# Optimization experiments

Measured on AMD Instinct MI355X. Metric: run time of the kernel, lower is better.

## Reference

```python
import jax, jax.numpy as jnp
import numpy as np

B, S, DIN, D, H, DK, FF, V, L = 4, 1024, 768, 224, 8, 28, 600, 8000, 8


def setup_inputs() -> dict:
    key = jax.random.key(0)
    ks = iter(jax.random.split(key, 32))
    g = lambda shape, s=0.02: jax.random.normal(next(ks), shape, jnp.float32) * s
    return {
        "x": jax.random.normal(next(ks), (B, S, DIN), jnp.float32),
        "Wp": g((DIN, D)), "bp": jnp.zeros((D,), jnp.float32),
        # per-layer stacked params, leading axis = L layers
        "Wq": g((L, H, D, DK)), "bq": jnp.zeros((L, H, DK), jnp.float32),
        "Wk": g((L, H, D, DK)), "bk": jnp.zeros((L, H, DK), jnp.float32),
        "Wv": g((L, H, D, DK)), "bv": jnp.zeros((L, H, DK), jnp.float32),
        "Wo": g((L, D, D)), "bo": jnp.zeros((L, D), jnp.float32),
        "W1": g((L, D, FF)), "b1": jnp.zeros((L, FF), jnp.float32),
        "W2": g((L, FF, FF)), "b2": jnp.zeros((L, FF), jnp.float32),
        "W3": g((L, FF, D)), "b3": jnp.zeros((L, D), jnp.float32),
        # LayerNorm over last TWO dims (seq, dmodel), one shared instance per layer
        "lnw": jnp.ones((L, S, D), jnp.float32), "lnb": jnp.zeros((L, S, D), jnp.float32),
        "Wf": g((D, V)), "bf": jnp.zeros((V,), jnp.float32),
    }


def _pos_enc(S_, D_):
    pos = jnp.arange(S_, dtype=jnp.float32)[:, None]          # [S,1]
    i = jnp.arange(D_, dtype=jnp.float32)[None, :]            # [1,D]
    ang = pos / jnp.power(jnp.float32(10000.0), 2.0 * i / D_)  # uses 2*i for BOTH
    return jnp.where(jnp.arange(D_)[None, :] % 2 == 0, jnp.sin(ang), jnp.cos(ang))


def _ln2d(x, w, b):
    # LayerNorm over last two dims (seq, dmodel), eps=1e-5
    mu = jnp.mean(x, axis=(-2, -1), keepdims=True)
    var = jnp.var(x, axis=(-2, -1), keepdims=True)
    return (x - mu) / jnp.sqrt(var + 1e-5) * w + b


def _attn(x, Wq, bq, Wk, bk, Wv, bv, Wo, bo):
    q = jnp.einsum('bsd,hdk->bhsk', x, Wq) + bq[:, None, :]
    k = jnp.einsum('bsd,hdk->bhsk', x, Wk) + bk[:, None, :]
    v = jnp.einsum('bsd,hdk->bhsk', x, Wv) + bv[:, None, :]
    scores = jnp.einsum('bhqk,bhsk->bhqs', q, k) / jnp.sqrt(jnp.float32(DK))
    causal = jnp.tril(jnp.ones((S, S), bool))
    scores = jnp.where(causal, scores, -jnp.inf)
    a = jax.nn.softmax(scores, axis=-1)
    o = jnp.einsum('bhqs,bhsk->bqhk', a, v).reshape(x.shape[0], S, D)
    return o @ Wo + bo + x  # residual inside attention (as in source)


def reference(x, Wp, bp, Wq, bq, Wk, bk, Wv, bv, Wo, bo,
              W1, b1, W2, b2, W3, b3, lnw, lnb, Wf, bf):
    h = x @ Wp + bp                      # proj_to_224: [B,S,224]
    h = h + _pos_enc(S, D)[None]         # positional encoding
    for l in range(L):
        h = _attn(h, Wq[l], bq[l], Wk[l], bk[l], Wv[l], bv[l], Wo[l], bo[l])
        h = _ln2d(h, lnw[l], lnb[l])
        f = jax.nn.relu(h @ W1[l] + b1[l])
        f = jax.nn.relu(f @ W2[l] + b2[l])
        f = f @ W3[l] + b3[l]
        h = _ln2d(f + h, lnw[l], lnb[l])  # feed_forward's LN (same params)
        h = _ln2d(h, lnw[l], lnb[l])      # outer LN (same params again)
    logits = (h @ Wf + bf) / 1.0          # temperature = 1.0
    return jax.nn.softmax(logits, axis=2)
```

## Files before the change

### kernel.cpp

```cpp
#include <hip/hip_runtime.h>
#include <math.h>

#define GF_BIAS   1
#define GF_RELU   2
#define GF_RESID  4
#define GF_POSENC 8
#define GF_F32OUT 16
#define GF_STAT6  32
#define GF_SWAP   64
#define GF_LNA    128
#define GF_LNA2   256
#define GF_LNRES  512
#define GF_LNRES2 1024

namespace {
constexpr int BB = 4, SS = 1024, DD = 224, FFF = 600, VV = 8000, LLl = 8;
constexpr int SD = SS * DD;
constexpr float INV_SD = 1.0f / (float)SD;

constexpr size_t WP   = 0;
constexpr size_t WQKV = WP + (size_t)256 * 768;
constexpr size_t WO   = WQKV + (size_t)LLl * 704 * 256;
constexpr size_t W1T  = WO + (size_t)LLl * 256 * 256;
constexpr size_t W2T  = W1T + (size_t)LLl * 640 * 256;
constexpr size_t W3T  = W2T + (size_t)LLl * 640 * 640;
constexpr size_t WFT  = W3T + (size_t)LLl * 256 * 640;
constexpr size_t HB   = WFT + (size_t)8064 * 256;
constexpr size_t H2B  = HB + (size_t)4096 * 256;
constexpr size_t OBUF = H2B + (size_t)4096 * 256;
constexpr size_t BIG  = OBUF + (size_t)4096 * 256;
constexpr size_t ENDB = BIG + (size_t)2 * 4096 * 640;
constexpr size_t FBYTE = ENDB * 2;
}

using short8 = __attribute__((ext_vector_type(8))) short;
using f32x4  = __attribute__((ext_vector_type(4))) float;

__device__ __forceinline__ float bits2f(unsigned u) {
  union { unsigned u; float f; } v; v.u = u; return v.f;
}
__device__ __forceinline__ unsigned short f2b(float f) {
  union { float f; unsigned u; } v; v.f = f;
  unsigned r = v.u + 0x7FFFu + ((v.u >> 16) & 1u);
  return (unsigned short)(r >> 16);
}
__device__ __forceinline__ float b2f(unsigned short b) {
  return bits2f((unsigned)b << 16);
}

__device__ __forceinline__ uint4 ln8(uint4 raw, const float* __restrict__ wp,
                                     const float* __restrict__ bp,
                                     float mu1, float rs1, float mu2, float rs2,
                                     bool dbl) {
  float4 w0 = *(const float4*)wp, w1v = *(const float4*)(wp + 4);
  float4 b0 = *(const float4*)bp, b1v = *(const float4*)(bp + 4);
  float wv[8] = {w0.x, w0.y, w0.z, w0.w, w1v.x, w1v.y, w1v.z, w1v.w};
  float bv[8] = {b0.x, b0.y, b0.z, b0.w, b1v.x, b1v.y, b1v.z, b1v.w};
  const unsigned* u = (const unsigned*)&raw;
  uint4 out;
  unsigned* ou = (unsigned*)&out;
#pragma unroll
  for (int q = 0; q < 4; ++q) {
    float x0 = bits2f(u[q] << 16), x1 = bits2f(u[q] & 0xFFFF0000u);
    float y0 = (x0 - mu1) * rs1 * wv[q * 2] + bv[q * 2];
    float y1 = (x1 - mu1) * rs1 * wv[q * 2 + 1] + bv[q * 2 + 1];
    if (dbl) {
      y0 = (y0 - mu2) * rs2 * wv[q * 2] + bv[q * 2];
      y1 = (y1 - mu2) * rs2 * wv[q * 2 + 1] + bv[q * 2 + 1];
    }
    ou[q] = (unsigned)f2b(y0) | ((unsigned)f2b(y1) << 16);
  }
  return out;
}

template <int BM, int BN, int FLAGS>
__global__ __launch_bounds__(256) void gemm_mfma(
    const unsigned short* __restrict__ A, const unsigned short* __restrict__ Bt,
    const float* __restrict__ bias, const unsigned short* __restrict__ Rz,
    void* __restrict__ Cout, int Kp, int N, int ldc,
    const float* __restrict__ lnwT, const float* __restrict__ lnbT,
    const float* __restrict__ stIn, const float* __restrict__ cst,
    const float* __restrict__ lnwS, const float* __restrict__ lnbS,
    float* __restrict__ statOut)
{
  constexpr bool HASLNA = (FLAGS & (GF_LNA | GF_LNA2)) != 0;
  constexpr bool HASLNR = (FLAGS & (GF_LNRES | GF_LNRES2)) != 0;
  constexpr bool DBLA = (FLAGS & GF_LNA2) != 0;
  constexpr bool DBLR = (FLAGS & GF_LNRES2) != 0;
  constexpr int MR = BM / 32, NR = BN / 32;
  constexpr int APT = BM / 32, BPT = BN / 32;
  constexpr int ABY = BM * 128, BBY = BN * 128;
  constexpr int CBY = (FLAGS & GF_F32OUT) ? (64 * (BN + 4) * 4) : (BM * (BN + 8) * 2);
  constexpr int SBY = (ABY + BBY) > CBY ? (ABY + BBY) : CBY;
  __shared__ __align__(16) char smem[SBY];
  __shared__ float red6[24];
  unsigned short* sA = (unsigned short*)smem;
  unsigned short* sB = (unsigned short*)(smem + ABY);
  const int t = threadIdx.x;
  const int l = t & 63;
  const int w = t >> 6, wr = w >> 1, wc = w & 1;
  const int m0 = ((FLAGS & GF_SWAP) ? blockIdx.x : blockIdx.y) * BM;
  const int n0 = ((FLAGS & GF_SWAP) ? blockIdx.y : blockIdx.x) * BN;
  const int nk = Kp >> 6;

  float mu1 = 0.f, rs1 = 1.f, mu2 = 0.f, rs2 = 1.f;
  if constexpr (HASLNA || HASLNR) {
    const float* st = stIn + (m0 >> 10) * 6;
    const float s0 = st[0], s1 = st[1];
    mu1 = s0 * INV_SD;
    rs1 = rsqrtf(s1 * INV_SD - mu1 * mu1 + 1e-5f);
    if constexpr (DBLA || DBLR) {
      const float swx = st[2], sw2x = st[3], sw2x2 = st[4], swbx = st[5];
      mu2 = (rs1 * (swx - mu1 * cst[0]) + cst[2]) * INV_SD;
      const float ey2 = (rs1 * rs1 * (sw2x2 - 2.f * mu1 * sw2x + mu1 * mu1 * cst[1]) +
                         2.f * rs1 * (swbx - mu1 * cst[4]) + cst[3]) * INV_SD;
      rs2 = rsqrtf(ey2 - mu2 * mu2 + 1e-5f);
    }
  }

  int aoff[APT], ar[APT], ac[APT];
#pragma unroll
  for (int p = 0; p < APT; ++p) {
    int off = (t + p * 256) * 16;
    int r = off >> 7;
    int cb = (off & 127) ^ ((r & 7) << 4);
    aoff[p] = off; ar[p] = r; ac[p] = cb >> 1;
  }
  int boff[BPT], br[BPT], bc[BPT];
#pragma unroll
  for (int p = 0; p < BPT; ++p) {
    int off = (t + p * 256) * 16;
    int r = off >> 7;
    int cb = (off & 127) ^ ((r & 7) << 4);
    boff[p] = off; br[p] = r; bc[p] = cb >> 1;
  }

  const unsigned short* Ab = A + (size_t)m0 * Kp;
  const unsigned short* Bb = Bt + (size_t)n0 * Kp;

  auto loadA = [&](int p, int kb) -> uint4 {
    const int d0 = kb + ac[p];
    uint4 raw = *(const uint4*)(Ab + (size_t)ar[p] * Kp + d0);
    if constexpr (HASLNA) {
      if (d0 >= DD) return make_uint4(0u, 0u, 0u, 0u);
      const int srow = (m0 + ar[p]) & (SS - 1);
      raw = ln8(raw, lnwT + (size_t)srow * DD + d0, lnbT + (size_t)srow * DD + d0,
                mu1, rs1, mu2, rs2, DBLA);
    }
    return raw;
  };

  uint4 ra[APT], rb[BPT];
#pragma unroll
  for (int p = 0; p < APT; ++p) ra[p] = loadA(p, 0);
#pragma unroll
  for (int p = 0; p < BPT; ++p) rb[p] = *(const uint4*)(Bb + (size_t)br[p] * Kp + bc[p]);

  f32x4 acc[MR][NR];
#pragma unroll
  for (int i = 0; i < MR; ++i)
#pragma unroll
    for (int j = 0; j < NR; ++j) acc[i][j] = {0.f, 0.f, 0.f, 0.f};

  for (int kt = 0; kt < nk; ++kt) {
#pragma unroll
    for (int p = 0; p < APT; ++p) *(uint4*)((char*)sA + aoff[p]) = ra[p];
#pragma unroll
    for (int p = 0; p < BPT; ++p) *(uint4*)((char*)sB + boff[p]) = rb[p];
    __syncthreads();
    if (kt + 1 < nk) {
      const int k1 = (kt + 1) * 64;
#pragma unroll
      for (int p = 0; p < APT; ++p) ra[p] = loadA(p, k1);
#pragma unroll
      for (int p = 0; p < BPT; ++p) rb[p] = *(const uint4*)(Bb + (size_t)br[p] * Kp + k1 + bc[p]);
    }
#pragma unroll
    for (int kh = 0; kh < 2; ++kh) {
      short8 af[MR], bfg[NR];
#pragma unroll
      for (int mi = 0; mi < MR; ++mi) {
        const int row = wr * (BM / 2) + mi * 16 + (l & 15);
        const int byte = (row * 128 + kh * 64 + (l >> 4) * 16) ^ ((row & 7) << 4);
        af[mi] = *(const short8*)((const char*)sA + byte);
      }
#pragma unroll
      for (int ni = 0; ni < NR; ++ni) {
        const int row = wc * (BN / 2) + ni * 16 + (l & 15);
        const int byte = (row * 128 + kh * 64 + (l >> 4) * 16) ^ ((row & 7) << 4);
        bfg[ni] = *(const short8*)((const char*)sB + byte);
      }
#pragma unroll
      for (int mi = 0; mi < MR; ++mi)
#pragma unroll
        for (int ni = 0; ni < NR; ++ni)
          acc[mi][ni] = __builtin_amdgcn_mfma_f32_16x16x32_bf16(af[mi], bfg[ni], acc[mi][ni], 0, 0, 0);
    }
    __syncthreads();
  }

  const int cl = l & 15, rl0 = (l >> 4) * 4;

  if constexpr ((FLAGS & GF_F32OUT) != 0) {
    constexpr int CST = BN + 4;
    float* Cs = (float*)smem;
    constexpr int NCH = BM / 64;
#pragma unroll
    for (int c = 0; c < NCH; ++c) {
      __syncthreads();
      if ((wr * (BM / 2)) / 64 == c) {
#pragma unroll
        for (int mi = 0; mi < MR; ++mi)
#pragma unroll
          for (int ni = 0; ni < NR; ++ni)
#pragma unroll
            for (int j = 0; j < 4; ++j) {
              const int rl = wr * (BM / 2) + mi * 16 + rl0 + j - c * 64;
              const int cc = wc * (BN / 2) + ni * 16 + cl;
              const int gn = n0 + cc;
              float v = acc[mi][ni][j];
              if ((FLAGS & GF_BIAS) && gn < N) v += bias[gn];
              Cs[rl * CST + cc] = v;
            }
      }
      __syncthreads();
      constexpr int CPR = BN / 4;
      constexpr int NIT = (64 * CPR) / 256;
#pragma unroll
      for (int i = 0; i < NIT; ++i) {
        const int ch = i * 256 + t;
        const int rr = ch / CPR, c4 = ch % CPR;
        const int gn = n0 + c4 * 4;
        const size_t gmr = (size_t)(m0 + c * 64 + rr);
        if (gn + 3 < N) {
          *(float4*)&((float*)Cout)[gmr * ldc + gn] = *(const float4*)&Cs[rr * CST + c4 * 4];
        } else {
#pragma unroll
          for (int c2 = 0; c2 < 4; ++c2)
            if (gn + c2 < N) ((float*)Cout)[gmr * ldc + gn + c2] = Cs[rr * CST + c4 * 4 + c2];
        }
      }
    }
  } else {
    constexpr int CST = BN + 8;
    unsigned short* Cs = (unsigned short*)smem;
    float ls0 = 0.f, ls1 = 0.f, ls2 = 0.f, ls3 = 0.f, ls4 = 0.f, ls5 = 0.f;
#pragma unroll
    for (int mi = 0; mi < MR; ++mi)
#pragma unroll
      for (int ni = 0; ni < NR; ++ni)
#pragma unroll
        for (int j = 0; j < 4; ++j) {
          const int rl = wr * (BM / 2) + mi * 16 + rl0 + j;
          const int cc = wc * (BN / 2) + ni * 16 + cl;
          const int gm = m0 + rl, gn = n0 + cc;
          const int srow = gm & (SS - 1);
          float v = acc[mi][ni][j];
          if ((FLAGS & GF_BIAS) && gn < N) v += bias[gn];
          if constexpr ((FLAGS & GF_RESID) != 0) {
            if constexpr (HASLNR) {
              if (gn < N) {
                float rv = b2f(Rz[(size_t)gm * ldc + gn]);
                const float wE = lnwT[(size_t)srow * DD + gn];
                const float bE = lnbT[(size_t)srow * DD + gn];
                rv = (rv - mu1) * rs1 * wE + bE;
                if constexpr (DBLR) rv = (rv - mu2) * rs2 * wE + bE;
                v += rv;
              }
            } else {
              v += b2f(Rz[(size_t)gm * ldc + gn]);
            }
          }
          if ((FLAGS & GF_POSENC) && gn < N) {
            float freq = expf(-(2.0f * gn / 224.0f) * 9.210340371976184f);
            float ang = (float)srow * freq;
            v += (gn & 1) ? cosf(ang) : sinf(ang);
          }
          if (FLAGS & GF_RELU) v = fmaxf(v, 0.f);
          if constexpr ((FLAGS & GF_STAT6) != 0) {
            if (gn < N) {
              const float wS = lnwS[(size_t)srow * DD + gn];
              const float bS = lnbS[(size_t)srow * DD + gn];
              const float wv = wS * v;
              ls0 += v; ls1 += v * v; ls2 += wv; ls3 += wS * wv;
              ls4 += wv * wv; ls5 += bS * wv;
            }
          }
          Cs[rl * CST + cc] = f2b(v);
        }
    __syncthreads();
#pragma unroll
    for (int it = 0; it < BM / 32; ++it) {
      const int rr = it * 32 + (t >> 3), qq = t & 7;
      const size_t gm = (size_t)(m0 + rr);
      *(uint4*)&((unsigned short*)Cout)[gm * ldc + n0 + qq * 8] =
          *(const uint4*)&Cs[rr * CST + qq * 8];
    }
    if constexpr ((FLAGS & GF_STAT6) != 0) {
      float s[6] = {ls0, ls1, ls2, ls3, ls4, ls5};
#pragma unroll
      for (int o2 = 32; o2 > 0; o2 >>= 1)
#pragma unroll
        for (int j = 0; j < 6; ++j) s[j] += __shfl_down(s[j], o2);
      if (l == 0)
#pragma unroll
        for (int j = 0; j < 6; ++j) red6[w * 6 + j] = s[j];
      __syncthreads();
      if (t < 6) {
        const float tot = red6[t] + red6[6 + t] + red6[12 + t] + red6[18 + t];
        atomicAdd(&statOut[(m0 >> 10) * 6 + t], tot);
      }
    }
  }
}

__global__ __launch_bounds__(512) void ffn_fused(
    const unsigned short* __restrict__ h2a,
    const unsigned short* __restrict__ W1t, const unsigned short* __restrict__ W2t,
    const unsigned short* __restrict__ W3t,
    const float* __restrict__ b1, const float* __restrict__ b2,
    const float* __restrict__ b3,
    const float* __restrict__ lnw, const float* __restrict__ lnb,
    const float* __restrict__ stA, float* __restrict__ statOut,
    unsigned short* __restrict__ Xout)
{
  __shared__ __align__(16) unsigned short sA[16 * 280];
  __shared__ __align__(16) unsigned short f1s[16 * 648];
  __shared__ __align__(16) unsigned short f2s[16 * 648];
  __shared__ float red6[48];
  const int t = threadIdx.x;
  const int l = t & 63, w = t >> 6;
  const int cl = l & 15, g8 = (l >> 4) * 8, rl0 = (l >> 4) * 4;
  const int m0 = blockIdx.x * 16;
  const float* st = stA + (m0 >> 10) * 6;
  const float mu1 = st[0] * INV_SD;
  const float rs1 = rsqrtf(st[1] * INV_SD - mu1 * mu1 + 1e-5f);

  {
    const int r = t >> 5, col = (t & 31) * 8;
    uint4 v = make_uint4(0u, 0u, 0u, 0u);
    if (col < DD) {
      const int srow = (m0 + r) & (SS - 1);
      uint4 raw = *(const uint4*)(h2a + (size_t)(m0 + r) * 256 + col);
      v = ln8(raw, lnw + (size_t)srow * DD + col, lnb + (size_t)srow * DD + col,
              mu1, rs1, 0.f, 1.f, false);
    }
    *(uint4*)(sA + r * 280 + col) = v;
  }
  __syncthreads();

  {
    f32x4 acc[5];
#pragma unroll
    for (int i = 0; i < 5; ++i) acc[i] = {0.f, 0.f, 0.f, 0.f};
    for (int ks = 0; ks < 8; ++ks) {
      const short8 af = *(const short8*)(sA + cl * 280 + ks * 32 + g8);
#pragma unroll
      for (int ni = 0; ni < 5; ++ni) {
        const int n = w * 80 + ni * 16 + cl;
        const short8 bf = *(const short8*)(W1t + (size_t)n * 256 + ks * 32 + g8);
        acc[ni] = __builtin_amdgcn_mfma_f32_16x16x32_bf16(af, bf, acc[ni], 0, 0, 0);
      }
    }
#pragma unroll
    for (int ni = 0; ni < 5; ++ni) {
      const int col = w * 80 + ni * 16 + cl;
      const float bias = (col < FFF) ? b1[col] : 0.f;
#pragma unroll
      for (int j = 0; j < 4; ++j)
        f1s[(rl0 + j) * 648 + col] = f2b(fmaxf(acc[ni][j] + bias, 0.f));
    }
  }
  __syncthreads();

  {
    f32x4 acc[5];
#pragma unroll
    for (int i = 0; i < 5; ++i) acc[i] = {0.f, 0.f, 0.f, 0.f};
    for (int ks = 0; ks < 20; ++ks) {
      const short8 af = *(const short8*)(f1s + cl * 648 + ks * 32 + g8);
#pragma unroll
      for (int ni = 0; ni < 5; ++ni) {
        const int n = w * 80 + ni * 16 + cl;
        const short8 bf = *(const short8*)(W2t + (size_t)n * 640 + ks * 32 + g8);
        acc[ni] = __builtin_amdgcn_mfma_f32_16x16x32_bf16(af, bf, acc[ni], 0, 0, 0);
      }
    }
#pragma unroll
    for (int ni = 0; ni < 5; ++ni) {
      const int col = w * 80 + ni * 16 + cl;
      const float bias = (col < FFF) ? b2[col] : 0.f;
#pragma unroll
      for (int j = 0; j < 4; ++j)
        f2s[(rl0 + j) * 648 + col] = f2b(fmaxf(acc[ni][j] + bias, 0.f));
    }
  }
  __syncthreads();

  float s6[6] = {0.f, 0.f, 0.f, 0.f, 0.f, 0.f};
  {
    f32x4 acc[2];
#pragma unroll
    for (int i = 0; i < 2; ++i) acc[i] = {0.f, 0.f, 0.f, 0.f};
    for (int ks = 0; ks < 20; ++ks) {
      const short8 af = *(const short8*)(f2s + cl * 648 + ks * 32 + g8);
#pragma unroll
      for (int ni = 0; ni < 2; ++ni) {
        const int n = w * 32 + ni * 16 + cl;
        const short8 bf = *(const short8*)(W3t + (size_t)n * 640 + ks * 32 + g8);
        acc[ni] = __builtin_amdgcn_mfma_f32_16x16x32_bf16(af, bf, acc[ni], 0, 0, 0);
      }
    }
    unsigned short* Cs = sA;
#pragma unroll
    for (int ni = 0; ni < 2; ++ni) {
      const int col = w * 32 + ni * 16 + cl;
      const float bias = (col < DD) ? b3[col] : 0.f;
#pragma unroll
      for (int j = 0; j < 4; ++j) {
        const int gm = m0 + rl0 + j;
        const int srow = gm & (SS - 1);
        float v = acc[ni][j] + bias;
        if (col < DD) {
          const float wE = lnw[(size_t)srow * DD + col];
          const float bE = lnb[(size_t)srow * DD + col];
          v += (b2f(h2a[(size_t)gm * 256 + col]) - mu1) * rs1 * wE + bE;
          const float wv = wE * v;
          s6[0] += v; s6[1] += v * v; s6[2] += wv; s6[3] += wE * wv;
          s6[4] += wv * wv; s6[5] += bE * wv;
        }
        Cs[(rl0 + j) * 280 + col] = f2b(v);
      }
    }
  }
#pragma unroll
  for (int o2 = 32; o2 > 0; o2 >>= 1)
#pragma unroll
    for (int j2 = 0; j2 < 6; ++j2) s6[j2] += __shfl_down(s6[j2], o2);
  if (l == 0)
#pragma unroll
    for (int j2 = 0; j2 < 6; ++j2) red6[w * 6 + j2] = s6[j2];
  __syncthreads();
  if (t < 6) {
    float tot = 0.f;
#pragma unroll
    for (int ww = 0; ww < 8; ++ww) tot += red6[ww * 6 + t];
    atomicAdd(&statOut[(m0 >> 10) * 6 + t], tot);
  }
  {
    const int r = t >> 5, col = (t & 31) * 8;
    *(uint4*)(Xout + (size_t)(m0 + r) * 256 + col) = *(const uint4*)(sA + r * 280 + col);
  }
}

__global__ __launch_bounds__(256) void ln2mat(
    const unsigned short* __restrict__ X, const float* __restrict__ lnw,
    const float* __restrict__ lnb, const float* __restrict__ st,
    const float* __restrict__ cst, unsigned short* __restrict__ Y)
{
  const int chunk = blockIdx.x * 256 + threadIdx.x;
  const int r = chunk >> 5, cc = chunk & 31;
  if (cc >= 28) {
    *(uint4*)(Y + (size_t)r * 256 + cc * 8) = make_uint4(0u, 0u, 0u, 0u);
    return;
  }
  const int b = r >> 10, srow = r & 1023;
  const float* s = st + b * 6;
  const float mu1 = s[0] * INV_SD;
  const float rs1 = rsqrtf(s[1] * INV_SD - mu1 * mu1 + 1e-5f);
  const float mu2 = (rs1 * (s[2] - mu1 * cst[0]) + cst[2]) * INV_SD;
  const float ey2 = (rs1 * rs1 * (s[4] - 2.f * mu1 * s[3] + mu1 * mu1 * cst[1]) +
                     2.f * rs1 * (s[5] - mu1 * cst[4]) + cst[3]) * INV_SD;
  const float rs2 = rsqrtf(ey2 - mu2 * mu2 + 1e-5f);
  uint4 raw = *(const uint4*)(X + (size_t)r * 256 + cc * 8);
  uint4 out = ln8(raw, lnw + (size_t)srow * DD + cc * 8, lnb + (size_t)srow * DD + cc * 8,
                  mu1, rs1, mu2, rs2, true);
  *(uint4*)(Y + (size_t)r * 256 + cc * 8) = out;
}

__device__ __forceinline__ void prep_wt2_body(
    const float* __restrict__ W, unsigned short* __restrict__ O,
    int K, int N, int Kp, int Np, size_t sW, size_t sO, int tile, int ll,
    float* __restrict__ T )
{
  const int tx = Np >> 5;
  const int tn = tile % tx, tk = tile / tx;
  const int n0 = tn * 32, k0 = tk * 32;
  const float* Wl = W + sW * ll;
  unsigned short* Ol = O + sO * ll;
  {
    const int r = threadIdx.x >> 3, c4 = (threadIdx.x & 7) * 4;
    const int k = k0 + r, n = n0 + c4;
    float4 v = make_float4(0.f, 0.f, 0.f, 0.f);
    if (k < K) {
      if (n + 3 < N) v = *(const float4*)&Wl[(size_t)k * N + n];
      else {
        if (n + 0 < N) v.x = Wl[(size_t)k * N + n + 0];
        if (n + 1 < N) v.y = Wl[(size_t)k * N + n + 1];
        if (n + 2 < N) v.z = Wl[(size_t)k * N + n + 2];
        if (n + 3 < N) v.w = Wl[(size_t)k * N + n + 3];
      }
    }
    *(float4*)&T[r * 36 + c4] = v;
  }
  __syncthreads();
  {
    const int nl = threadIdx.x >> 3, k4 = (threadIdx.x & 7) * 4;
    ushort4 u;
    u.x = f2b(T[(k4 + 0) * 36 + nl]); u.y = f2b(T[(k4 + 1) * 36 + nl]);
    u.z = f2b(T[(k4 + 2) * 36 + nl]); u.w = f2b(T[(k4 + 3) * 36 + nl]);
    *(ushort4*)&Ol[(size_t)(n0 + nl) * Kp + k0 + k4] = u;
  }
}

__global__ __launch_bounds__(256) void prep_weights(
    const float* __restrict__ Wp, const float* __restrict__ Wo,
    const float* __restrict__ W1, const float* __restrict__ W2,
    const float* __restrict__ W3, const float* __restrict__ Wf,
    const float* __restrict__ lnw, const float* __restrict__ lnb,
    unsigned short* __restrict__ wpT, unsigned short* __restrict__ woT,
    unsigned short* __restrict__ w1T, unsigned short* __restrict__ w2T,
    unsigned short* __restrict__ w3T, unsigned short* __restrict__ wfT,
    float* __restrict__ cst)
{
  __shared__ float T[32 * 36];
  const int b = blockIdx.x;
  if (b < 192) {
    prep_wt2_body(Wp, wpT, 768, 224, 768, 256, 0, 0, b, 0, T);
  } else if (b < 704) {
    const int f = b - 192;
    prep_wt2_body(Wo, woT, 224, 224, 256, 256, (size_t)224 * 224, (size_t)256 * 256,
                  f % 64, f / 64, T);
  } else if (b < 1984) {
    const int f = b - 704;
    prep_wt2_body(W1, w1T, 224, 600, 256, 640, (size_t)224 * 600, (size_t)640 * 256,
                  f % 160, f / 160, T);
  } else if (b < 5184) {
    const int f = b - 1984;
    prep_wt2_body(W2, w2T, 600, 600, 640, 640, (size_t)600 * 600, (size_t)640 * 640,
                  f % 400, f / 400, T);
  } else if (b < 6464) {
    const int f = b - 5184;
    prep_wt2_body(W3, w3T, 600, 224, 640, 256, (size_t)600 * 224, (size_t)256 * 640,
                  f % 160, f / 160, T);
  } else if (b < 8480) {
    prep_wt2_body(Wf, wfT, 224, 8000, 256, 8064, 0, 0, b - 6464, 0, T);
  } else {
    const int f = b - 8480;
    const int g = f & 63, ll = f >> 6;
    const float* wv = lnw + (size_t)ll * SD + g * 3584;
    const float* bv = lnb + (size_t)ll * SD + g * 3584;
    float s[5] = {0.f, 0.f, 0.f, 0.f, 0.f};
    for (int c = threadIdx.x * 4; c < 3584; c += 1024) {
      float4 w4 = *(const float4*)(wv + c);
      float4 b4 = *(const float4*)(bv + c);
      const float* wf2 = (const float*)&w4;
// ... 170 lines not shown
    const int row = qbase + g * 4 + jj;
    unsigned short* op = o + ((size_t)(b * SS + row)) * 256 + h * 28;
    op[cl] = f2b(o0[jj] * inv);
    if (cl < 12) op[16 + cl] = f2b(o1[jj] * inv);
  }
}

__global__ __launch_bounds__(256) void softmax_rows(float* __restrict__ logits)
{
  const int row = blockIdx.x;
  float* p = logits + (size_t)row * VV;
  __shared__ float4 buf[VV / 4];
  __shared__ float red[4];
  const int tid = threadIdx.x;

  float mx = -INFINITY;
  for (int i = tid; i < VV / 4; i += 256) {
    float4 v = *(const float4*)(p + i * 4);
    buf[i] = v;
    mx = fmaxf(fmaxf(fmaxf(mx, v.x), fmaxf(v.y, v.z)), v.w);
  }
#pragma unroll
  for (int o2 = 32; o2 > 0; o2 >>= 1) mx = fmaxf(mx, __shfl_down(mx, o2));
  if ((tid & 63) == 0) red[tid >> 6] = mx;
  __syncthreads();
  mx = fmaxf(fmaxf(red[0], red[1]), fmaxf(red[2], red[3]));
  __syncthreads();

  float s = 0.f;
  for (int i = tid; i < VV / 4; i += 256) {
    float4 v = buf[i];
    v.x = __expf(v.x - mx); v.y = __expf(v.y - mx);
    v.z = __expf(v.z - mx); v.w = __expf(v.w - mx);
    buf[i] = v;
    s += v.x + v.y + v.z + v.w;
  }
#pragma unroll
  for (int o2 = 32; o2 > 0; o2 >>= 1) s += __shfl_down(s, o2);
  if ((tid & 63) == 0) red[tid >> 6] = s;
  __syncthreads();
  s = red[0] + red[1] + red[2] + red[3];
  const float inv = 1.0f / s;
  for (int i = tid; i < VV / 4; i += 256) {
    float4 v = buf[i];
    v.x *= inv; v.y *= inv; v.z *= inv; v.w *= inv;
    *(float4*)(p + i * 4) = v;
  }
}

extern "C" void kernel_launch(void* const* d_in, const int* in_sizes, int n_in,
                              void* d_out, int out_size, void* d_ws, size_t ws_size,
                              hipStream_t stream) {
  const float* x   = (const float*)d_in[0];
  const float* Wp  = (const float*)d_in[1];
  const float* bp  = (const float*)d_in[2];
  const float* Wq  = (const float*)d_in[3];
  const float* bq  = (const float*)d_in[4];
  const float* Wk  = (const float*)d_in[5];
  const float* bk  = (const float*)d_in[6];
  const float* Wv  = (const float*)d_in[7];
  const float* bv  = (const float*)d_in[8];
  const float* Wo  = (const float*)d_in[9];
  const float* bo  = (const float*)d_in[10];
  const float* W1  = (const float*)d_in[11];
  const float* b1  = (const float*)d_in[12];
  const float* W2  = (const float*)d_in[13];
  const float* b2  = (const float*)d_in[14];
  const float* W3  = (const float*)d_in[15];
  const float* b3  = (const float*)d_in[16];
  const float* lnw = (const float*)d_in[17];
  const float* lnb = (const float*)d_in[18];
  const float* Wf  = (const float*)d_in[19];
  const float* bf  = (const float*)d_in[20];

  unsigned short* wsb = (unsigned short*)d_ws;
  unsigned short* wpT   = wsb + WP;
  unsigned short* wqkvT = wsb + WQKV;
  unsigned short* woT   = wsb + WO;
  unsigned short* w1T   = wsb + W1T;
  unsigned short* w2T   = wsb + W2T;
  unsigned short* w3T   = wsb + W3T;
  unsigned short* wfT   = wsb + WFT;
  unsigned short* X     = wsb + HB;
  unsigned short* h2a   = wsb + H2B;
  unsigned short* obuf  = wsb + OBUF;
  unsigned short* xb    = wsb + BIG;
  unsigned short* qkvb  = wsb + BIG;
  float* bcat  = (float*)((char*)d_ws + FBYTE);
  float* stats = bcat + LLl * 672;
  float* cstA  = stats + 384;

  hipMemsetAsync(wqkvT, 0, (size_t)LLl * 704 * 256 * 2, stream);
  prep_x<<<3072, 256, 0, stream>>>(x, xb, stats);
  prep_wqkv<<<1568, 256, 0, stream>>>(Wq, Wk, Wv, bq, bk, bv, wqkvT, bcat);
  prep_weights<<<8992, 256, 0, stream>>>(Wp, Wo, W1, W2, W3, Wf, lnw, lnb,
                                         wpT, woT, w1T, w2T, w3T, wfT, cstA);

  gemm_mfma<32, 64, GF_BIAS | GF_POSENC><<<dim3(4, 128), 256, 0, stream>>>(
      xb, wpT, bp, nullptr, X, 768, 224, 256,
      nullptr, nullptr, nullptr, nullptr, nullptr, nullptr, nullptr);

  for (int l = 0; l < LLl; ++l) {
    float* stA = stats + (size_t)(2 * l) * 24;
    float* stB = stats + (size_t)(2 * l + 1) * 24;
    const float* stPrev = stats + (size_t)(2 * l - 1) * 24;
    const float* lnwP = lnw + (size_t)(l - 1) * SD;
    const float* lnbP = lnb + (size_t)(l - 1) * SD;
    const float* cstP = cstA + (l - 1) * 5;
    const float* lnwL = lnw + (size_t)l * SD;
    const float* lnbL = lnb + (size_t)l * SD;

    if (l == 0) {
      gemm_mfma<64, 64, GF_BIAS><<<dim3(11, 64), 256, 0, stream>>>(
          X, wqkvT, bcat, nullptr, qkvb, 256, 672, 704,
          nullptr, nullptr, nullptr, nullptr, nullptr, nullptr, nullptr);
    } else {
      gemm_mfma<64, 64, GF_BIAS | GF_LNA2><<<dim3(11, 64), 256, 0, stream>>>(
          X, wqkvT + (size_t)l * 704 * 256, bcat + l * 672, nullptr, qkvb, 256, 672, 704,
          lnwP, lnbP, stPrev, cstP, nullptr, nullptr, nullptr);
    }
    attn_mfma<<<dim3(BB * 8, SS / 64), 256, 0, stream>>>(qkvb, obuf);
    if (l == 0) {
      gemm_mfma<32, 64, GF_BIAS | GF_RESID | GF_STAT6><<<dim3(4, 128), 256, 0, stream>>>(
          obuf, woT, bo, X, h2a, 256, 224, 256,
          nullptr, nullptr, nullptr, nullptr, lnwL, lnbL, stA);
    } else {
      gemm_mfma<32, 64, GF_BIAS | GF_RESID | GF_LNRES2 | GF_STAT6>
          <<<dim3(4, 128), 256, 0, stream>>>(
          obuf, woT + (size_t)l * 256 * 256, bo + (size_t)l * 224, X, h2a, 256, 224, 256,
          lnwP, lnbP, stPrev, cstP, lnwL, lnbL, stA);
    }
    ffn_fused<<<256, 512, 0, stream>>>(
        h2a, w1T + (size_t)l * 640 * 256, w2T + (size_t)l * 640 * 640,
        w3T + (size_t)l * 256 * 640, b1 + (size_t)l * 600, b2 + (size_t)l * 600,
        b3 + (size_t)l * 224, lnwL, lnbL, stA, stB, X);
  }

  ln2mat<<<512, 256, 0, stream>>>(X, lnw + (size_t)7 * SD, lnb + (size_t)7 * SD,
                                  stats + (size_t)15 * 24, cstA + 7 * 5, h2a);
  gemm_mfma<128, 128, GF_BIAS | GF_F32OUT | GF_SWAP><<<dim3(32, 63), 256, 0, stream>>>(
      h2a, wfT, bf, nullptr, (float*)d_out, 256, 8000, 8000,
      nullptr, nullptr, nullptr, nullptr, nullptr, nullptr, nullptr);
  softmax_rows<<<4096, 256, 0, stream>>>((float*)d_out);
}
```

Baseline: 1.250 ms.

## Fuse out-projection, FFN and next-layer QKV into one cooperative kernel per layer

Replaces the per-layer out-projection GEMM, the FFN kernel and the next layer's QKV GEMM with a single cooperative kernel. It uses grid-wide syncs to wait for the LayerNorm statistics between stages, and keeps the intermediate h2a tile in shared memory instead of global memory. This removes two kernel launches per layer and a global round trip of the intermediate activation. In exchange, 256 blocks of 512 threads must be co-resident, each grid.sync costs a barrier, and the out-projection and QKV stages run on only 16-row tiles with weights read straight from global memory.

Measured after the change: 1.722 ms. 1.38x slower.

```diff
diff --git a/kernel.cpp b/kernel.cpp
--- a/kernel.cpp
+++ b/kernel.cpp
@@ -1,17 +1,15 @@
 #include <hip/hip_runtime.h>
+#include <hip/hip_cooperative_groups.h>
 #include <math.h>
+
+namespace cg = cooperative_groups;
 
 #define GF_BIAS   1
 #define GF_RELU   2
 #define GF_RESID  4
 #define GF_POSENC 8
 #define GF_F32OUT 16
-#define GF_STAT6  32
 #define GF_SWAP   64
-#define GF_LNA    128
-#define GF_LNA2   256
-#define GF_LNRES  512
-#define GF_LNRES2 1024
 
 namespace {
 constexpr int BB = 4, SS = 1024, DD = 224, FFF = 600, VV = 8000, LLl = 8;
@@ -73,27 +71,29 @@
   return out;
 }
 
+__device__ __forceinline__ void ln2stats(const float* __restrict__ st,
+                                         const float* __restrict__ cst,
+                                         float& mu1, float& rs1, float& mu2, float& rs2)
+{
+  mu1 = st[0] * INV_SD;
+  rs1 = rsqrtf(st[1] * INV_SD - mu1 * mu1 + 1e-5f);
+  mu2 = (rs1 * (st[2] - mu1 * cst[0]) + cst[2]) * INV_SD;
+  const float ey2 = (rs1 * rs1 * (st[4] - 2.f * mu1 * st[3] + mu1 * mu1 * cst[1]) +
+                     2.f * rs1 * (st[5] - mu1 * cst[4]) + cst[3]) * INV_SD;
+  rs2 = rsqrtf(ey2 - mu2 * mu2 + 1e-5f);
+}
+
 template <int BM, int BN, int FLAGS>
 __global__ __launch_bounds__(256) void gemm_mfma(
     const unsigned short* __restrict__ A, const unsigned short* __restrict__ Bt,
-    const float* __restrict__ bias, const unsigned short* __restrict__ Rz,
-    void* __restrict__ Cout, int Kp, int N, int ldc,
-    const float* __restrict__ lnwT, const float* __restrict__ lnbT,
-    const float* __restrict__ stIn, const float* __restrict__ cst,
-    const float* __restrict__ lnwS, const float* __restrict__ lnbS,
-    float* __restrict__ statOut)
+    const float* __restrict__ bias, void* __restrict__ Cout, int Kp, int N, int ldc)
 {
-  constexpr bool HASLNA = (FLAGS & (GF_LNA | GF_LNA2)) != 0;
-  constexpr bool HASLNR = (FLAGS & (GF_LNRES | GF_LNRES2)) != 0;
-  constexpr bool DBLA = (FLAGS & GF_LNA2) != 0;
-  constexpr bool DBLR = (FLAGS & GF_LNRES2) != 0;
   constexpr int MR = BM / 32, NR = BN / 32;
   constexpr int APT = BM / 32, BPT = BN / 32;
   constexpr int ABY = BM * 128, BBY = BN * 128;
   constexpr int CBY = (FLAGS & GF_F32OUT) ? (64 * (BN + 4) * 4) : (BM * (BN + 8) * 2);
   constexpr int SBY = (ABY + BBY) > CBY ? (ABY + BBY) : CBY;
   __shared__ __align__(16) char smem[SBY];
-  __shared__ float red6[24];
   unsigned short* sA = (unsigned short*)smem;
   unsigned short* sB = (unsigned short*)(smem + ABY);
   const int t = threadIdx.x;
@@ -103,21 +103,6 @@
   const int n0 = ((FLAGS & GF_SWAP) ? blockIdx.y : blockIdx.x) * BN;
   const int nk = Kp >> 6;
 
-  float mu1 = 0.f, rs1 = 1.f, mu2 = 0.f, rs2 = 1.f;
-  if constexpr (HASLNA || HASLNR) {
-    const float* st = stIn + (m0 >> 10) * 6;
-    const float s0 = st[0], s1 = st[1];
-    mu1 = s0 * INV_SD;
-    rs1 = rsqrtf(s1 * INV_SD - mu1 * mu1 + 1e-5f);
-    if constexpr (DBLA || DBLR) {
-      const float swx = st[2], sw2x = st[3], sw2x2 = st[4], swbx = st[5];
-      mu2 = (rs1 * (swx - mu1 * cst[0]) + cst[2]) * INV_SD;
-      const float ey2 = (rs1 * rs1 * (sw2x2 - 2.f * mu1 * sw2x + mu1 * mu1 * cst[1]) +
-                         2.f * rs1 * (swbx - mu1 * cst[4]) + cst[3]) * INV_SD;
-      rs2 = rsqrtf(ey2 - mu2 * mu2 + 1e-5f);
-    }
-  }
-
   int aoff[APT], ar[APT], ac[APT];
 #pragma unroll
   for (int p = 0; p < APT; ++p) {
@@ -138,21 +123,9 @@
   const unsigned short* Ab = A + (size_t)m0 * Kp;
   const unsigned short* Bb = Bt + (size_t)n0 * Kp;
 
-  auto loadA = [&](int p, int kb) -> uint4 {
-    const int d0 = kb + ac[p];
-    uint4 raw = *(const uint4*)(Ab + (size_t)ar[p] * Kp + d0);
-    if constexpr (HASLNA) {
-      if (d0 >= DD) return make_uint4(0u, 0u, 0u, 0u);
-      const int srow = (m0 + ar[p]) & (SS - 1);
-      raw = ln8(raw, lnwT + (size_t)srow * DD + d0, lnbT + (size_t)srow * DD + d0,
-                mu1, rs1, mu2, rs2, DBLA);
-    }
-    return raw;
-  };
-
   uint4 ra[APT], rb[BPT];
 #pragma unroll
-  for (int p = 0; p < APT; ++p) ra[p] = loadA(p, 0);
+  for (int p = 0; p < APT; ++p) ra[p] = *(const uint4*)(Ab + (size_t)ar[p] * Kp + ac[p]);
 #pragma unroll
   for (int p = 0; p < BPT; ++p) rb[p] = *(const uint4*)(Bb + (size_t)br[p] * Kp + bc[p]);
 
@@ -171,7 +144,7 @@
     if (kt + 1 < nk) {
       const int k1 = (kt + 1) * 64;
 #pragma unroll
-      for (int p = 0; p < APT; ++p) ra[p] = loadA(p, k1);
+      for (int p = 0; p < APT; ++p) ra[p] = *(const uint4*)(Ab + (size_t)ar[p] * Kp + k1 + ac[p]);
 #pragma unroll
       for (int p = 0; p < BPT; ++p) rb[p] = *(const uint4*)(Bb + (size_t)br[p] * Kp + k1 + bc[p]);
     }
@@ -244,7 +217,6 @@
   } else {
     constexpr int CST = BN + 8;
     unsigned short* Cs = (unsigned short*)smem;
-    float ls0 = 0.f, ls1 = 0.f, ls2 = 0.f, ls3 = 0.f, ls4 = 0.f, ls5 = 0.f;
 #pragma unroll
     for (int mi = 0; mi < MR; ++mi)
 #pragma unroll
@@ -257,35 +229,11 @@
           const int srow = gm & (SS - 1);
           float v = acc[mi][ni][j];
           if ((FLAGS & GF_BIAS) && gn < N) v += bias[gn];
-          if constexpr ((FLAGS & GF_RESID) != 0) {
-            if constexpr (HASLNR) {
-              if (gn < N) {
-                float rv = b2f(Rz[(size_t)gm * ldc + gn]);
-                const float wE = lnwT[(size_t)srow * DD + gn];
-                const float bE = lnbT[(size_t)srow * DD + gn];
-                rv = (rv - mu1) * rs1 * wE + bE;
-                if constexpr (DBLR) rv = (rv - mu2) * rs2 * wE + bE;
-                v += rv;
-              }
-            } else {
-              v += b2f(Rz[(size_t)gm * ldc + gn]);
-            }
-          }
           if ((FLAGS & GF_POSENC) && gn < N) {
             float freq = expf(-(2.0f * gn / 224.0f) * 9.210340371976184f);
             float ang = (float)srow * freq;
             v += (gn & 1) ? cosf(ang) : sinf(ang);
           }
-          if (FLAGS & GF_RELU) v = fmaxf(v, 0.f);
-          if constexpr ((FLAGS & GF_STAT6) != 0) {
-            if (gn < N) {
-              const float wS = lnwS[(size_t)srow * DD + gn];
-              const float bS = lnbS[(size_t)srow * DD + gn];
-              const float wv = wS * v;
-              ls0 += v; ls1 += v * v; ls2 += wv; ls3 += wS * wv;
-              ls4 += wv * wv; ls5 += bS * wv;
-            }
-          }
           Cs[rl * CST + cc] = f2b(v);
         }
     __syncthreads();
@@ -296,160 +244,269 @@
       *(uint4*)&((unsigned short*)Cout)[gm * ldc + n0 + qq * 8] =
           *(const uint4*)&Cs[rr * CST + qq * 8];
     }
-    if constexpr ((FLAGS & GF_STAT6) != 0) {
-      float s[6] = {ls0, ls1, ls2, ls3, ls4, ls5};
-#pragma unroll
-      for (int o2 = 32; o2 > 0; o2 >>= 1)
-#pragma unroll
-        for (int j = 0; j < 6; ++j) s[j] += __shfl_down(s[j], o2);
-      if (l == 0)
-#pragma unroll
-        for (int j = 0; j < 6; ++j) red6[w * 6 + j] = s[j];
-      __syncthreads();
-      if (t < 6) {
-        const float tot = red6[t] + red6[6 + t] + red6[12 + t] + red6[18 + t];
-        atomicAdd(&statOut[(m0 >> 10) * 6 + t], tot);
-      }
-    }
-  }
-}
-
-__global__ __launch_bounds__(512) void ffn_fused(
-    const unsigned short* __restrict__ h2a,
+  }
+}
+
+__global__ __launch_bounds__(512) void layer_tail(
+    const unsigned short* __restrict__ obuf, unsigned short* __restrict__ X,
+    unsigned short* __restrict__ qkvb,
+    const unsigned short* __restrict__ woT, const float* __restrict__ bo,
     const unsigned short* __restrict__ W1t, const unsigned short* __restrict__ W2t,
     const unsigned short* __restrict__ W3t,
     const float* __restrict__ b1, const float* __restrict__ b2,
     const float* __restrict__ b3,
-    const float* __restrict__ lnw, const float* __restrict__ lnb,
-    const float* __restrict__ stA, float* __restrict__ statOut,
-    unsigned short* __restrict__ Xout)
+    const unsigned short* __restrict__ wqN, const float* __restrict__ bcN,
+    const float* __restrict__ lnwP, const float* __restrict__ lnbP,
+    const float* __restrict__ cstP, const float* __restrict__ stPrev,
+    const float* __restrict__ lnwL, const float* __restrict__ lnbL,
+    const float* __restrict__ cstL,
+    float* __restrict__ stA, float* __restrict__ stB,
+    int isL0, int hasQkv)
 {
-  __shared__ __align__(16) unsigned short sA[16 * 280];
-  __shared__ __align__(16) unsigned short f1s[16 * 648];
-  __shared__ __align__(16) unsigned short f2s[16 * 648];
-  __shared__ float red6[48];
+  cg::grid_group grid = cg::this_grid();
+  __shared__ __align__(16) char smem[59584];
+  unsigned short* oS   = (unsigned short*)smem;
+  unsigned short* sAx  = (unsigned short*)smem;
+  unsigned short* h2aL = (unsigned short*)(smem + 8960);
+  unsigned short* f1s  = (unsigned short*)(smem + 17920);
+  unsigned short* f2s  = (unsigned short*)(smem + 38656);
+  unsigned short* qS   = (unsigned short*)(smem + 17920);
+  float* red6 = (float*)(smem + 59392);
+
   const int t = threadIdx.x;
   const int l = t & 63, w = t >> 6;
   const int cl = l & 15, g8 = (l >> 4) * 8, rl0 = (l >> 4) * 4;
   const int m0 = blockIdx.x * 16;
-  const float* st = stA + (m0 >> 10) * 6;
-  const float mu1 = st[0] * INV_SD;
-  const float rs1 = rsqrtf(st[1] * INV_SD - mu1 * mu1 + 1e-5f);
+  const int batch = m0 >> 10;
+
+  float mu1 = 0.f, rs1 = 1.f, mu2 = 0.f, rs2 = 1.f;
+  if (!isL0) ln2stats(stPrev + batch * 6, cstP, mu1, rs1, mu2, rs2);
 
   {
     const int r = t >> 5, col = (t & 31) * 8;
-    uint4 v = make_uint4(0u, 0u, 0u, 0u);
-    if (col < DD) {
-      const int srow = (m0 + r) & (SS - 1);
-      uint4 raw = *(const uint4*)(h2a + (size_t)(m0 + r) * 256 + col);
-      v = ln8(raw, lnw + (size_t)srow * DD + col, lnb + (size_t)srow * DD + col,
-              mu1, rs1, 0.f, 1.f, false);
-    }
-    *(uint4*)(sA + r * 280 + col) = v;
+    *(uint4*)(oS + r * 280 + col) = *(const uint4*)(obuf + (size_t)(m0 + r) * 256 + col);
   }
   __syncthreads();
 
-  {
-    f32x4 acc[5];
-#pragma unroll
-    for (int i = 0; i < 5; ++i) acc[i] = {0.f, 0.f, 0.f, 0.f};
-    for (int ks = 0; ks < 8; ++ks) {
-      const short8 af = *(const short8*)(sA + cl * 280 + ks * 32 + g8);
-#pragma unroll
-      for (int ni = 0; ni < 5; ++ni) {
-        const int n = w * 80 + ni * 16 + cl;
-        const short8 bf = *(const short8*)(W1t + (size_t)n * 256 + ks * 32 + g8);
-        acc[ni] = __builtin_amdgcn_mfma_f32_16x16x32_bf16(af, bf, acc[ni], 0, 0, 0);
-      }
-    }
-#pragma unroll
-    for (int ni = 0; ni < 5; ++ni) {
-      const int col = w * 80 + ni * 16 + cl;
-      const float bias = (col < FFF) ? b1[col] : 0.f;
-#pragma unroll
-      for (int j = 0; j < 4; ++j)
-        f1s[(rl0 + j) * 648 + col] = f2b(fmaxf(acc[ni][j] + bias, 0.f));
-    }
-  }
-  __syncthreads();
-
-  {
-    f32x4 acc[5];
-#pragma unroll
-    for (int i = 0; i < 5; ++i) acc[i] = {0.f, 0.f, 0.f, 0.f};
-    for (int ks = 0; ks < 20; ++ks) {
-      const short8 af = *(const short8*)(f1s + cl * 648 + ks * 32 + g8);
-#pragma unroll
-      for (int ni = 0; ni < 5; ++ni) {
-        const int n = w * 80 + ni * 16 + cl;
-        const short8 bf = *(const short8*)(W2t + (size_t)n * 640 + ks * 32 + g8);
-        acc[ni] = __builtin_amdgcn_mfma_f32_16x16x32_bf16(af, bf, acc[ni], 0, 0, 0);
-      }
-    }
-#pragma unroll
-    for (int ni = 0; ni < 5; ++ni) {
-      const int col = w * 80 + ni * 16 + cl;
-      const float bias = (col < FFF) ? b2[col] : 0.f;
-#pragma unroll
-      for (int j = 0; j < 4; ++j)
-        f2s[(rl0 + j) * 648 + col] = f2b(fmaxf(acc[ni][j] + bias, 0.f));
-    }
-  }
-  __syncthreads();
-
-  float s6[6] = {0.f, 0.f, 0.f, 0.f, 0.f, 0.f};
   {
     f32x4 acc[2];
 #pragma unroll
     for (int i = 0; i < 2; ++i) acc[i] = {0.f, 0.f, 0.f, 0.f};
-    for (int ks = 0; ks < 20; ++ks) {
-      const short8 af = *(const short8*)(f2s + cl * 648 + ks * 32 + g8);
+    for (int ks = 0; ks < 8; ++ks) {
+      const short8 af = *(const short8*)(oS + cl * 280 + ks * 32 + g8);
 #pragma unroll
       for (int ni = 0; ni < 2; ++ni) {
         const int n = w * 32 + ni * 16 + cl;
-        const short8 bf = *(const short8*)(W3t + (size_t)n * 640 + ks * 32 + g8);
+        const short8 bf = *(const short8*)(woT + (size_t)n * 256 + ks * 32 + g8);
         acc[ni] = __builtin_amdgcn_mfma_f32_16x16x32_bf16(af, bf, acc[ni], 0, 0, 0);
       }
     }
-    unsigned short* Cs = sA;
+    float s6[6] = {0.f, 0.f, 0.f, 0.f, 0.f, 0.f};
 #pragma unroll
     for (int ni = 0; ni < 2; ++ni) {
       const int col = w * 32 + ni * 16 + cl;
-      const float bias = (col < DD) ? b3[col] : 0.f;
 #pragma unroll
       for (int j = 0; j < 4; ++j) {
         const int gm = m0 + rl0 + j;
         const int srow = gm & (SS - 1);
-        float v = acc[ni][j] + bias;
+        float v = acc[ni][j];
         if (col < DD) {
-          const float wE = lnw[(size_t)srow * DD + col];
-          const float bE = lnb[(size_t)srow * DD + col];
-          v += (b2f(h2a[(size_t)gm * 256 + col]) - mu1) * rs1 * wE + bE;
-          const float wv = wE * v;
-          s6[0] += v; s6[1] += v * v; s6[2] += wv; s6[3] += wE * wv;
-          s6[4] += wv * wv; s6[5] += bE * wv;
+          v += bo[col];
+          float rv = b2f(X[(size_t)gm * 256 + col]);
+          if (!isL0) {
+            const float wE = lnwP[(size_t)srow * DD + col];
+            const float bE = lnbP[(size_t)srow * DD + col];
+            rv = (rv - mu1) * rs1 * wE + bE;
+            rv = (rv - mu2) * rs2 * wE + bE;
+          }
+          v += rv;
+          const float wS = lnwL[(size_t)srow * DD + col];
+          const float bS = lnbL[(size_t)srow * DD + col];
+          const float wv = wS * v;
+          s6[0] += v; s6[1] += v * v; s6[2] += wv; s6[3] += wS * wv;
+          s6[4] += wv * wv; s6[5] += bS * wv;
         }
-        Cs[(rl0 + j) * 280 + col] = f2b(v);
-      }
-    }
-  }
-#pragma unroll
-  for (int o2 = 32; o2 > 0; o2 >>= 1)
-#pragma unroll
-    for (int j2 = 0; j2 < 6; ++j2) s6[j2] += __shfl_down(s6[j2], o2);
-  if (l == 0)
-#pragma unroll
-    for (int j2 = 0; j2 < 6; ++j2) red6[w * 6 + j2] = s6[j2];
-  __syncthreads();
-  if (t < 6) {
-    float tot = 0.f;
-#pragma unroll
-    for (int ww = 0; ww < 8; ++ww) tot += red6[ww * 6 + t];
-    atomicAdd(&statOut[(m0 >> 10) * 6 + t], tot);
-  }
+        h2aL[(rl0 + j) * 280 + col] = f2b(v);
+      }
+    }
+#pragma unroll
+    for (int o2 = 32; o2 > 0; o2 >>= 1)
+#pragma unroll
+      for (int j2 = 0; j2 < 6; ++j2) s6[j2] += __shfl_down(s6[j2], o2);
+    if (l == 0)
+#pragma unroll
+      for (int j2 = 0; j2 < 6; ++j2) red6[w * 6 + j2] = s6[j2];
+    __syncthreads();
+    if (t < 6) {
+      float tot = 0.f;
+#pragma unroll
+      for (int ww = 0; ww < 8; ++ww) tot += red6[ww * 6 + t];
+      atomicAdd(&stA[batch * 6 + t], tot);
+    }
+  }
+
+  grid.sync();
+
   {
-    const int r = t >> 5, col = (t & 31) * 8;
-    *(uint4*)(Xout + (size_t)(m0 + r) * 256 + col) = *(const uint4*)(sA + r * 280 + col);
+    const float* sa = stA + batch * 6;
+    const float muF = sa[0] * INV_SD;
+    const float rsF = rsqrtf(sa[1] * INV_SD - muF * muF + 1e-5f);
+
+    {
+      const int r = t >> 5, col = (t & 31) * 8;
+      uint4 v = make_uint4(0u, 0u, 0u, 0u);
+      if (col < DD) {
+        const int srow = (m0 + r) & (SS - 1);
+        uint4 raw = *(const uint4*)(h2aL + r * 280 + col);
+        v = ln8(raw, lnwL + (size_t)srow * DD + col, lnbL + (size_t)srow * DD + col,
+                muF, rsF, 0.f, 1.f, false);
+      }
+      *(uint4*)(sAx + r * 280 + col) = v;
+    }
+    __syncthreads();
+
+    {
+      f32x4 acc[5];
+#pragma unroll
+      for (int i = 0; i < 5; ++i) acc[i] = {0.f, 0.f, 0.f, 0.f};
+      for (int ks = 0; ks < 8; ++ks) {
+        const short8 af = *(const short8*)(sAx + cl * 280 + ks * 32 + g8);
+#pragma unroll
+        for (int ni = 0; ni < 5; ++ni) {
+          const int n = w * 80 + ni * 16 + cl;
+          const short8 bf = *(const short8*)(W1t + (size_t)n * 256 + ks * 32 + g8);
+          acc[ni] = __builtin_amdgcn_mfma_f32_16x16x32_bf16(af, bf, acc[ni], 0, 0, 0);
+        }
+      }
+#pragma unroll
+      for (int ni = 0; ni < 5; ++ni) {
+        const int col = w * 80 + ni * 16 + cl;
+        const float bias = (col < FFF) ? b1[col] : 0.f;
+#pragma unroll
+        for (int j = 0; j < 4; ++j)
+          f1s[(rl0 + j) * 648 + col] = f2b(fmaxf(acc[ni][j] + bias, 0.f));
+      }
+    }
+    __syncthreads();
+
+    {
+      f32x4 acc[5];
+#pragma unroll
+      for (int i = 0; i < 5; ++i) acc[i] = {0.f, 0.f, 0.f, 0.f};
+      for (int ks = 0; ks < 20; ++ks) {
+        const short8 af = *(const short8*)(f1s + cl * 648 + ks * 32 + g8);
+#pragma unroll
+        for (int ni = 0; ni < 5; ++ni) {
+          const int n = w * 80 + ni * 16 + cl;
+          const short8 bf = *(const short8*)(W2t + (size_t)n * 640 + ks * 32 + g8);
+          acc[ni] = __builtin_amdgcn_mfma_f32_16x16x32_bf16(af, bf, acc[ni], 0, 0, 0);
+        }
+      }
+#pragma unroll
+      for (int ni = 0; ni < 5; ++ni) {
+        const int col = w * 80 + ni * 16 + cl;
+        const float bias = (col < FFF) ? b2[col] : 0.f;
+#pragma unroll
+        for (int j = 0; j < 4; ++j)
+          f2s[(rl0 + j) * 648 + col] = f2b(fmaxf(acc[ni][j] + bias, 0.f));
+      }
+    }
+    __syncthreads();
+
+    float s6[6] = {0.f, 0.f, 0.f, 0.f, 0.f, 0.f};
+    {
+      f32x4 acc[2];
+#pragma unroll
+      for (int i = 0; i < 2; ++i) acc[i] = {0.f, 0.f, 0.f, 0.f};
+      for (int ks = 0; ks < 20; ++ks) {
+        const short8 af = *(const short8*)(f2s + cl * 648 + ks * 32 + g8);
+#pragma unroll
+        for (int ni = 0; ni < 2; ++ni) {
+          const int n = w * 32 + ni * 16 + cl;
+          const short8 bf = *(const short8*)(W3t + (size_t)n * 640 + ks * 32 + g8);
+          acc[ni] = __builtin_amdgcn_mfma_f32_16x16x32_bf16(af, bf, acc[ni], 0, 0, 0);
+        }
+      }
+#pragma unroll
+      for (int ni = 0; ni < 2; ++ni) {
+        const int col = w * 32 + ni * 16 + cl;
+        const float bias = (col < DD) ? b3[col] : 0.f;
+#pragma unroll
+        for (int j = 0; j < 4; ++j) {
+          const int gm = m0 + rl0 + j;
+          const int srow = gm & (SS - 1);
+          float v = acc[ni][j] + bias;
+          if (col < DD) {
+            const float wE = lnwL[(size_t)srow * DD + col];
+            const float bE = lnbL[(size_t)srow * DD + col];
+            v += (b2f(h2aL[(rl0 + j) * 280 + col]) - muF) * rsF * wE + bE;
+            const float wv = wE * v;
+            s6[0] += v; s6[1] += v * v; s6[2] += wv; s6[3] += wE * wv;
+            s6[4] += wv * wv; s6[5] += bE * wv;
+          }
+          sAx[(rl0 + j) * 280 + col] = f2b(v);
+        }
+      }
+    }
+#pragma unroll
+    for (int o2 = 32; o2 > 0; o2 >>= 1)
+#pragma unroll
+      for (int j2 = 0; j2 < 6; ++j2) s6[j2] += __shfl_down(s6[j2], o2);
+    if (l == 0)
+#pragma unroll
+      for (int j2 = 0; j2 < 6; ++j2) red6[w * 6 + j2] = s6[j2];
+    __syncthreads();
+    if (t < 6) {
+      float tot = 0.f;
+#pragma unroll
+      for (int ww = 0; ww < 8; ++ww) tot += red6[ww * 6 + t];
+      atomicAdd(&stB[batch * 6 + t], tot);
+    }
+    {
+      const int r = t >> 5, col = (t & 31) * 8;
+      *(uint4*)(X + (size_t)(m0 + r) * 256 + col) = *(const uint4*)(sAx + r * 280 + col);
+    }
+  }
+
+  if (!hasQkv) return;
+  grid.sync();
+
+  {
+    float m1, r1, m2, r2;
+    ln2stats(stB + batch * 6, cstL, m1, r1, m2, r2);
+    short8 af2[8];
+    const int srowA = (m0 + cl) & (SS - 1);
+#pragma unroll
+    for (int ks = 0; ks < 8; ++ks) {
+      const int d0 = ks * 32 + g8;
+      uint4 tr = make_uint4(0u, 0u, 0u, 0u);
+      if (d0 < DD) {
+        uint4 raw = *(const uint4*)(sAx + cl * 280 + d0);
+        tr = ln8(raw, lnwL + (size_t)srowA * DD + d0, lnbL + (size_t)srowA * DD + d0,
+                 m1, r1, m2, r2, true);
+      }
+      af2[ks] = *(const short8*)&tr;
+    }
+    __syncthreads();
+    for (int idx = w; idx < 44; idx += 8) {
+      f32x4 acc = {0.f, 0.f, 0.f, 0.f};
+      const int nbase = idx * 16;
+#pragma unroll
+      for (int ks = 0; ks < 8; ++ks) {
+        const short8 bf = *(const short8*)(wqN + (size_t)(nbase + cl) * 256 + ks * 32 + g8);
+        acc = __builtin_amdgcn_mfma_f32_16x16x32_bf16(af2[ks], bf, acc, 0, 0, 0);
+      }
+      const int col = nbase + cl;
+      const float bb = (col < 672) ? bcN[col] : 0.f;
+#pragma unroll
+      for (int j = 0; j < 4; ++j)
+        qS[(rl0 + j) * 712 + col] = f2b(acc[j] + bb);
+    }
+    __syncthreads();
+    for (int c = t; c < 1408; c += 512) {
+      const int r = c / 88, q8 = (c % 88) * 8;
+      *(uint4*)(qkvb + (size_t)(m0 + r) * 704 + q8) = *(const uint4*)(qS + r * 712 + q8);
+    }
   }
 }
 
@@ -465,13 +522,8 @@
     return;
   }
   const int b = r >> 10, srow = r & 1023;
-  const float* s = st + b * 6;
-  const float mu1 = s[0] * INV_SD;
-  const float rs1 = rsqrtf(s[1] * INV_SD - mu1 * mu1 + 1e-5f);
-  const float mu2 = (rs1 * (s[2] - mu1 * cst[0]) + cst[2]) * INV_SD;
-  const float ey2 = (rs1 * rs1 * (s[4] - 2.f * mu1 * s[3] + mu1 * mu1 * cst[1]) +
-                     2.f * rs1 * (s[5] - mu1 * cst[4]) + cst[3]) * INV_SD;
-  const float rs2 = rsqrtf(ey2 - mu2 * mu2 + 1e-5f);
+  float mu1, rs1, mu2, rs2;
+  ln2stats(st + b * 6, cst, mu1, rs1, mu2, rs2);
   uint4 raw = *(const uint4*)(X + (size_t)r * 256 + cc * 8);
   uint4 out = ln8(raw, lnw + (size_t)srow * DD + cc * 8, lnb + (size_t)srow * DD + cc * 8,
                   mu1, rs1, mu2, rs2, true);
@@ -808,7 +860,7 @@
   unsigned short* w3T   = wsb + W3T;
   unsigned short* wfT   = wsb + WFT;
   unsigned short* X     = wsb + HB;
-  unsigned short* h2a   = wsb + H2B;
+  unsigned short* hF    = wsb + H2B;
   unsigned short* obuf  = wsb + OBUF;
   unsigned short* xb    = wsb + BIG;
   unsigned short* qkvb  = wsb + BIG;
@@ -823,49 +875,51 @@
                                          wpT, woT, w1T, w2T, w3T, wfT, cstA);
 
   gemm_mfma<32, 64, GF_BIAS | GF_POSENC><<<dim3(4, 128), 256, 0, stream>>>(
-      xb, wpT, bp, nullptr, X, 768, 224, 256,
-      nullptr, nullptr, nullptr, nullptr, nullptr, nullptr, nullptr);
+      xb, wpT, bp, X, 768, 224, 256);
+  gemm_mfma<64, 64, GF_BIAS><<<dim3(11, 64), 256, 0, stream>>>(
+      X, wqkvT, bcat, qkvb, 256, 672, 704);
 
   for (int l = 0; l < LLl; ++l) {
-    float* stA = stats + (size_t)(2 * l) * 24;
-    float* stB = stats + (size_t)(2 * l + 1) * 24;
-    const float* stPrev = stats + (size_t)(2 * l - 1) * 24;
-    const float* lnwP = lnw + (size_t)(l - 1) * SD;
-    const float* lnbP = lnb + (size_t)(l - 1) * SD;
-    const float* cstP = cstA + (l - 1) * 5;
-    const float* lnwL = lnw + (size_t)l * SD;
-    const float* lnbL = lnb + (size_t)l * SD;
-
-    if (l == 0) {
-      gemm_mfma<64, 64, GF_BIAS><<<dim3(11, 64), 256, 0, stream>>>(
-          X, wqkvT, bcat, nullptr, qkvb, 256, 672, 704,
-          nullptr, nullptr, nullptr, nullptr, nullptr, nullptr, nullptr);
-    } else {
-      gemm_mfma<64, 64, GF_BIAS | GF_LNA2><<<dim3(11, 64), 256, 0, stream>>>(
-          X, wqkvT + (size_t)l * 704 * 256, bcat + l * 672, nullptr, qkvb, 256, 672, 704,
-          lnwP, lnbP, stPrev, cstP, nullptr, nullptr, nullptr);
-    }
     attn_mfma<<<dim3(BB * 8, SS / 64), 256, 0, stream>>>(qkvb, obuf);
-    if (l == 0) {
-      gemm_mfma<32, 64, GF_BIAS | GF_RESID | GF_STAT6><<<dim3(4, 128), 256, 0, stream>>>(
-          obuf, woT, bo, X, h2a, 256, 224, 256,
-          nullptr, nullptr, nullptr, nullptr, lnwL, lnbL, stA);
-    } else {
-      gemm_mfma<32, 64, GF_BIAS | GF_RESID | GF_LNRES2 | GF_STAT6>
-          <<<dim3(4, 128), 256, 0, stream>>>(
-          obuf, woT + (size_t)l * 256 * 256, bo + (size_t)l * 224, X, h2a, 256, 224, 256,
-          lnwP, lnbP, stPrev, cstP, lnwL, lnbL, stA);
-    }
-    ffn_fused<<<256, 512, 0, stream>>>(
-        h2a, w1T + (size_t)l * 640 * 256, w2T + (size_t)l * 640 * 640,
-        w3T + (size_t)l * 256 * 640, b1 + (size_t)l * 600, b2 + (size_t)l * 600,
-        b3 + (size_t)l * 224, lnwL, lnbL, stA, stB, X);
+
+    const unsigned short* p_obuf = obuf;
+    unsigned short* p_X = X;
+    unsigned short* p_qkvb = qkvb;
+    const unsigned short* p_woT = woT + (size_t)l * 256 * 256;
+    const float* p_bo = bo + (size_t)l * 224;
+    const unsigned short* p_w1T = w1T + (size_t)l * 640 * 256;
+    const unsigned short* p_w2T = w2T + (size_t)l * 640 * 640;
+    const unsigned short* p_w3T = w3T + (size_t)l * 256 * 640;
+    const float* p_b1 = b1 + (size_t)l * 600;
+    const float* p_b2 = b2 + (size_t)l * 600;
+    const float* p_b3 = b3 + (size_t)l * 224;
+    const int ln_ = (l + 1 < LLl) ? l + 1 : 0;
+    const unsigned short* p_wq = wqkvT + (size_t)ln_ * 704 * 256;
+    const float* p_bc = bcat + (size_t)ln_ * 672;
+    const int lp = (l > 0) ? l - 1 : 0;
+    const float* p_lnwP = lnw + (size_t)lp * SD;
+    const float* p_lnbP = lnb + (size_t)lp * SD;
+    const float* p_cstP = cstA + lp * 5;
+    const float* p_stPrev = stats + (size_t)((l > 0) ? 2 * l - 1 : 0) * 24;
+    const float* p_lnwL = lnw + (size_t)l * SD;
+    const float* p_lnbL = lnb + (size_t)l * SD;
+    const float* p_cstL = cstA + l * 5;
+    float* p_stA = stats + (size_t)(2 * l) * 24;
+    float* p_stB = stats + (size_t)(2 * l + 1) * 24;
+    int isL0 = (l == 0) ? 1 : 0;
+    int hasQkv = (l < LLl - 1) ? 1 : 0;
+
+    void* args[] = {&p_obuf, &p_X, &p_qkvb, &p_woT, &p_bo,
+                    &p_w1T, &p_w2T, &p_w3T, &p_b1, &p_b2, &p_b3,
+                    &p_wq, &p_bc, &p_lnwP, &p_lnbP, &p_cstP, &p_stPrev,
+                    &p_lnwL, &p_lnbL, &p_cstL, &p_stA, &p_stB, &isL0, &hasQkv};
+    hipLaunchCooperativeKernel((void*)layer_tail, dim3(256), dim3(512),
+                               args, 0, stream);
   }
 
   ln2mat<<<512, 256, 0, stream>>>(X, lnw + (size_t)7 * SD, lnb + (size_t)7 * SD,
-                                  stats + (size_t)15 * 24, cstA + 7 * 5, h2a);
+                                  stats + (size_t)15 * 24, cstA + 7 * 5, hF);
   gemm_mfma<128, 128, GF_BIAS | GF_F32OUT | GF_SWAP><<<dim3(32, 63), 256, 0, stream>>>(
-      h2a, wfT, bf, nullptr, (float*)d_out, 256, 8000, 8000,
-      nullptr, nullptr, nullptr, nullptr, nullptr, nullptr, nullptr);
+      hF, wfT, bf, (float*)d_out, 256, 8000, 8000);
   softmax_rows<<<4096, 256, 0, stream>>>((float*)d_out);
 }
```
